# Optimization experiments

Measured on AMD Instinct MI355X. Metric: run time of the kernel, lower is better.

Reference implementation:

```python
import jax, jax.numpy as jnp
import numpy as np

KSIZE = 15
SIGMA = 3.0
PAD = KSIZE // 2


def _gauss_kernel2d():
    g = jnp.arange(KSIZE, dtype=jnp.float32) - KSIZE // 2
    g = jnp.exp(-(g ** 2) / (2.0 * SIGMA * SIGMA))
    g = g / g.sum()
    return g[:, None] * g[None, :]  # [15,15]


def _depthwise_blur(x, k2):
    # x: [B,C,H,W]; 15x15 Gaussian applied per channel (matches per-channel F.conv2d loop)
    C = x.shape[1]
    kernel = jnp.broadcast_to(k2[None, None], (C, 1, KSIZE, KSIZE))
    return jax.lax.conv_general_dilated(
        x, kernel, window_strides=(1, 1), padding=[(PAD, PAD), (PAD, PAD)],
        feature_group_count=C, dimension_numbers=("NCHW", "OIHW", "NCHW"))


def setup_inputs() -> dict:
    key = jax.random.key(0)
    B, C, H, W = 4, 3, 1024, 1024
    x = jax.random.uniform(key, (B, C, H, W), dtype=jnp.float32)
    f32 = lambda v: jnp.asarray(v, dtype=jnp.float32)
    return {
        "x": x,
        "gains": jnp.array([1.1, 1.0, 0.9], dtype=jnp.float32),
        "gamma": f32(0.9),
        "shadow_boost": f32(0.1),
        "highlight_reduce": f32(0.1),
        "brightness": f32(0.05),
        "contrast": f32(1.1),
        "enhance_amount": f32(0.8),
        "softness": f32(0.6),
        "intensity": f32(0.3),
        "rotation": f32(30.0),
        "hardness": f32(2.0),
    }


def reference(x, gains, gamma, shadow_boost, highlight_reduce, brightness,
              contrast, enhance_amount, softness, intensity, rotation, hardness):
    B, C, H, W = x.shape
    k2 = _gauss_kernel2d()

    # WhiteBalanceAdjustment
    x = x * gains.reshape(1, C, 1, 1)
    # ToneCurveAdjustment
    x = jnp.power(x, gamma)
    # ShadowHighlightEnhancement
    hi = jax.nn.sigmoid((x - 0.5) * 10.0)
    x = jnp.clip(x + shadow_boost * (1.0 - hi) - highlight_reduce * hi, 0.0, 1.0)
    # GlobalBrightnessContrastAdjustment
    x = jnp.clip(contrast * (x - 0.5) + 0.5 + brightness, 0.0, 1.0)
    # LocalContrastEnhancement
    local_mean = _depthwise_blur(x, k2)
    x = x + enhance_amount * (x - local_mean)
    # SoftnessFilter
    blurred = _depthwise_blur(x, k2)
    x = softness * blurred + (1.0 - softness) * x
    # GradientNDAdjustment
    ys = jnp.linspace(-1.0, 1.0, H, dtype=jnp.float32)
    xs = jnp.linspace(-1.0, 1.0, W, dtype=jnp.float32)
    grid_y, grid_x = jnp.meshgrid(ys, xs, indexing="ij")
    theta = rotation * (np.pi / 180.0)
    grid_rot = grid_x * jnp.cos(theta) + grid_y * jnp.sin(theta)
    mask = jax.nn.sigmoid(-hardness * grid_rot)[None, None]  # [1,1,H,W]
    x = jnp.clip(x * (1.0 - intensity * mask), 0.0, 1.0)

    return jnp.clip(x, 0.0, 1.0)
```

## Files before the change

### kernel.cpp

```cpp
#include <hip/hip_runtime.h>
#include <math.h>

#define HH 1024
#define WW 1024
#define NPLANES 12
#define PLANE (HH * WW)

#define TW 64
#define TH 64
#define RROWS 92
#define PA 96
#define PB 80
#define P1 80
#define PC 64

struct W15 { float w[15]; };

__device__ inline float chain1(float t, float gain, float gamma, float sb,
                               float hr, float br, float ct) {
    t = t * gain;
    t = __builtin_amdgcn_exp2f(gamma * __log2f(t));
    float hi = __fdividef(1.0f, 1.0f + __expf((0.5f - t) * 10.0f));
    t = t + sb * (1.0f - hi) - hr * hi;
    t = fminf(fmaxf(t, 0.0f), 1.0f);
    t = ct * (t - 0.5f) + 0.5f + br;
    return fminf(fmaxf(t, 0.0f), 1.0f);
}

__device__ inline float4 hdot4(const float* f, const W15& wk) {
    float4 o; float* po = (float*)&o;
#pragma unroll
    for (int j = 0; j < 4; ++j) {
        float a = 0.0f, b = 0.0f;
#pragma unroll
        for (int k = 0; k < 8; ++k)  a += wk.w[k] * f[j + 1 + k];
#pragma unroll
        for (int k = 8; k < 15; ++k) b += wk.w[k] * f[j + 1 + k];
        po[j] = a + b;
    }
    return o;
}

__device__ inline float dot15(const float* win, const W15& wk) {
    float a = 0.0f, b = 0.0f;
#pragma unroll
    for (int k = 0; k < 8; ++k)  a += wk.w[k] * win[k];
#pragma unroll
    for (int k = 8; k < 15; ++k) b += wk.w[k] * win[k];
    return a + b;
}

__device__ inline void tile_map(int& p, int& x0, int& y0, bool& edge) {
    int L = (blockIdx.z * gridDim.y + blockIdx.y) * gridDim.x + blockIdx.x;
    int xcd = L & 7;
    int t   = L >> 3;
    int g   = xcd * 384 + t;
    p = g >> 8;
    int w  = g & 255;
    int ty = w >> 4, tx = w & 15;
    x0 = tx * TW; y0 = ty * TH;
    edge = (tx == 0) || (tx == 15) || (ty == 0) || (ty == 15);
}

__global__ __launch_bounds__(256) void k_fused(
    const float* __restrict__ x, float* __restrict__ dst,
    const float* __restrict__ gains,
    const float* __restrict__ pg, const float* __restrict__ psb,
    const float* __restrict__ phr, const float* __restrict__ pbr,
    const float* __restrict__ pct, const float* __restrict__ penh,
    const float* __restrict__ psoft, const float* __restrict__ pint,
    const float* __restrict__ prot, const float* __restrict__ phard,
    W15 wk)
{
    __shared__ float A [RROWS * PA];
    __shared__ float Bb[RROWS * PB];

    int p, x0, y0; bool edge;
    tile_map(p, x0, y0, edge);
    const int tid = threadIdx.x;
    const int tx  = tid & 63;
    const int ty  = tid >> 6;

    const float* __restrict__ plane = x + (size_t)p * PLANE;
    const float gain  = gains[p % 3];
    const float gamma = *pg, sb = *psb, hr = *phr, br = *pbr, ct = *pct;

    if (!edge) {
        const float* base = plane + (size_t)(y0 - 14) * WW + (x0 - 16);
        auto do1 = [&](int c) {
            int r = c / 24, c4 = c % 24;
            float4 v = *(const float4*)(base + (size_t)r * WW + 4 * c4);
            float* pv = (float*)&v;
#pragma unroll
            for (int q = 0; q < 4; ++q)
                pv[q] = chain1(pv[q], gain, gamma, sb, hr, br, ct);
            *(float4*)&A[r * PA + ((c4 ^ (r & 7)) << 2)] = v;
        };
#pragma unroll
        for (int it = 0; it < 8; ++it) do1(tid + 256 * it);
        if (tid < 160) do1(tid + 2048);
    } else {
        auto do1e = [&](int c) {
            int r = c / 24, c4 = c % 24;
            int gy  = y0 - 14 + r;
            int gx0 = x0 - 16 + 4 * c4;
            float4 v = make_float4(0.f, 0.f, 0.f, 0.f);
            if ((unsigned)gy < HH) {
                const float* row = plane + (size_t)gy * WW;
                float* pv = (float*)&v;
                if (gx0 >= 0 && gx0 + 3 < WW) {
                    v = *(const float4*)(row + gx0);
#pragma unroll
                    for (int q = 0; q < 4; ++q)
                        pv[q] = chain1(pv[q], gain, gamma, sb, hr, br, ct);
                } else {
#pragma unroll
                    for (int q = 0; q < 4; ++q) {
                        int gx = gx0 + q;
                        if ((unsigned)gx < WW)
                            pv[q] = chain1(row[gx], gain, gamma, sb, hr, br, ct);
                    }
                }
            }
            *(float4*)&A[r * PA + ((c4 ^ (r & 7)) << 2)] = v;
        };
#pragma unroll
        for (int it = 0; it < 8; ++it) do1e(tid + 256 * it);
        if (tid < 160) do1e(tid + 2048);
    }
    __syncthreads();

    float cc[16];
#pragma unroll
    for (int j = 0; j < 16; ++j) {
        int rr = ty * 16 + j + 14;
        cc[j] = A[rr * PA + ((((tx >> 2) + 4) ^ (rr & 7)) << 2) + (tx & 3)];
    }
    {
        auto do2 = [&](int c) {
            int r = c / 20, j4 = c % 20;
            int rx = r & 7;
            float f[20];
#pragma unroll
            for (int i = 0; i < 5; ++i)
                *(float4*)&f[4 * i] =
                    *(const float4*)&A[r * PA + (((j4 + i) ^ rx) << 2)];
            *(float4*)&Bb[r * PB + 4 * j4] = hdot4(f, wk);
        };
#pragma unroll
        for (int it = 0; it < 7; ++it) do2(tid + 256 * it);
        if (tid < 48) do2(tid + 1792);
    }
    __syncthreads();

    float* B1 = A;
    if (tid < 240) {
        int j    = tid % 80;
        int band = tid / 80;
        int r1s  = band * 26;
        bool xin = (unsigned)(x0 - 8 + j) < WW;
        float win[15];
#pragma unroll
        for (int k = 0; k < 14; ++k) win[k] = Bb[(r1s + k) * PB + j];
#pragma unroll
        for (int jj = 0; jj < 26; ++jj) {
            win[14] = Bb[(r1s + jj + 14) * PB + j];
            float v = dot15(win, wk);
            if (edge) {
                int gy = y0 - 7 + r1s + jj;
                if (!((unsigned)gy < HH) || !xin) v = 0.0f;
            }
            B1[(r1s + jj) * P1 + j] = v;
#pragma unroll
            for (int k = 0; k < 14; ++k) win[k] = win[k + 1];
        }
    }
    __syncthreads();

    float bb[16];
#pragma unroll
    for (int j = 0; j < 16; ++j)
        bb[j] = B1[(ty * 16 + j + 7) * P1 + (tx + 8)];
    float* C = Bb;
    {
        auto do4 = [&](int c) {
            int r = c >> 4, j4 = c & 15;
            float f[20];
#pragma unroll
            for (int i = 0; i < 5; ++i)
                *(float4*)&f[4 * i] = *(const float4*)&B1[r * P1 + 4 * (j4 + i)];
            *(float4*)&C[r * PC + 4 * j4] = hdot4(f, wk);
        };
#pragma unroll
        for (int it = 0; it < 4; ++it) do4(tid + 256 * it);
        if (tid < 224) do4(tid + 1024);
    }
    __syncthreads();

    const float e     = *penh;
    const float s     = *psoft;
    const float inten = *pint;
    const float hard  = *phard;
    const float theta = (*prot) * 0.017453292519943295f;
    const float cth = __cosf(theta), sth = __sinf(theta);
    const int   gx    = x0 + tx;
    const float gbase = (-1.0f + 2.0f * (float)gx * (1.0f / (float)(WW - 1))) * cth;
    const float ce    = 1.0f + e;

    float win[15];
#pragma unroll
    for (int k = 0; k < 14; ++k) win[k] = C[(ty * 16 + k) * PC + tx];

    float* __restrict__ dstP = dst + (size_t)p * PLANE;
#pragma unroll
    for (int jj = 0; jj < 16; ++jj) {
        win[14] = C[(ty * 16 + jj + 14) * PC + tx];
        float B2  = dot15(win, wk);
        float x2c = ce * cc[jj] - e * bb[jj];
        float bx2 = ce * bb[jj] - e * B2;
        float v   = s * bx2 + (1.0f - s) * x2c;
        int   y   = y0 + ty * 16 + jj;
        float gyn = -1.0f + 2.0f * (float)y * (1.0f / (float)(HH - 1));
        float mask = __fdividef(1.0f, 1.0f + __expf(hard * (gbase + gyn * sth)));
        v = v * (1.0f - inten * mask);
        v = fminf(fmaxf(v, 0.0f), 1.0f);
        dstP[(size_t)y * WW + gx] = v;
#pragma unroll
        for (int k = 0; k < 14; ++k) win[k] = win[k + 1];
    }
}

extern "C" void kernel_launch(void* const* d_in, const int* in_sizes, int n_in,
                              void* d_out, int out_size, void* d_ws, size_t ws_size,
                              hipStream_t stream)
{
    const float* x       = (const float*)d_in[0];
    const float* gains   = (const float*)d_in[1];
    const float* p_gamma = (const float*)d_in[2];
    const float* p_sb    = (const float*)d_in[3];
    const float* p_hr    = (const float*)d_in[4];
    const float* p_br    = (const float*)d_in[5];
    const float* p_ct    = (const float*)d_in[6];
    const float* p_enh   = (const float*)d_in[7];
    const float* p_soft  = (const float*)d_in[8];
    const float* p_int   = (const float*)d_in[9];
    const float* p_rot   = (const float*)d_in[10];
    const float* p_hard  = (const float*)d_in[11];

    W15 wk;
    {
        double g[15], sum = 0.0;
        for (int i = 0; i < 15; ++i) { double d = (double)(i - 7); g[i] = exp(-d * d / 18.0); sum += g[i]; }
        for (int i = 0; i < 15; ++i) wk.w[i] = (float)(g[i] / sum);
    }

    dim3 grid(WW / TW, HH / TH, NPLANES);
    k_fused<<<grid, dim3(256), 0, stream>>>(
        x, (float*)d_out, gains, p_gamma, p_sb, p_hr, p_br, p_ct,
        p_enh, p_soft, p_int, p_rot, p_hard, wk);
}
```

Measured before the change: 202.6 us.

## Fuse input load with horizontal blur in registers and shrink LDS staging

Each thread now loads a 32-wide strip of a row straight from global memory, applies the tone chain and computes 16 horizontal blur outputs in registers. Only the horizontally blurred result goes to shared memory, so the full pre-blur tile is no longer staged there and one barrier disappears. The centre values are reloaded from global and the tone chain recomputed for them, and the second horizontal pass also processes 16 outputs per thread. Shared memory drops to one combined, swizzled buffer, which may raise occupancy. The cost is redundant global loads, repeated tone-chain evaluation on halo columns, and higher register pressure from the 32-float strips.

```diff
diff --git a/kernel.cpp b/kernel.cpp
--- a/kernel.cpp
+++ b/kernel.cpp
@@ -8,11 +8,9 @@
 
 #define TW 64
 #define TH 64
-#define RROWS 92
-#define PA 96
-#define PB 80
-#define P1 80
-#define PC 64
+#define RH 92
+#define RB 78
+#define PH 80
 
 struct W15 { float w[15]; };
 
@@ -27,18 +25,21 @@
     return fminf(fmaxf(t, 0.0f), 1.0f);
 }
 
-__device__ inline float4 hdot4(const float* f, const W15& wk) {
-    float4 o; float* po = (float*)&o;
-#pragma unroll
-    for (int j = 0; j < 4; ++j) {
+__device__ inline int hq(int r, int q) { return r * PH + ((q ^ (r & 3)) << 2); }
+__device__ inline int hs(int r, int j) {
+    return r * PH + ((((j >> 2) ^ (r & 3)) << 2) | (j & 3));
+}
+
+__device__ inline void dot16(const float* f, const W15& wk, float* o) {
+#pragma unroll
+    for (int j = 0; j < 16; ++j) {
         float a = 0.0f, b = 0.0f;
 #pragma unroll
         for (int k = 0; k < 8; ++k)  a += wk.w[k] * f[j + 1 + k];
 #pragma unroll
         for (int k = 8; k < 15; ++k) b += wk.w[k] * f[j + 1 + k];
-        po[j] = a + b;
-    }
-    return o;
+        o[j] = a + b;
+    }
 }
 
 __device__ inline float dot15(const float* win, const W15& wk) {
@@ -72,8 +73,9 @@
     const float* __restrict__ prot, const float* __restrict__ phard,
     W15 wk)
 {
-    __shared__ float A [RROWS * PA];
-    __shared__ float Bb[RROWS * PB];
+    __shared__ float lds[(RH + RB) * PH];
+    float* Hs  = lds;
+    float* B1s = lds + RH * PH;
 
     int p, x0, y0; bool edge;
     tile_map(p, x0, y0, edge);
@@ -85,120 +87,96 @@
     const float gain  = gains[p % 3];
     const float gamma = *pg, sb = *psb, hr = *phr, br = *pbr, ct = *pct;
 
-    if (!edge) {
-        const float* base = plane + (size_t)(y0 - 14) * WW + (x0 - 16);
-        auto do1 = [&](int c) {
-            int r = c / 24, c4 = c % 24;
-            float4 v = *(const float4*)(base + (size_t)r * WW + 4 * c4);
-            float* pv = (float*)&v;
-#pragma unroll
-            for (int q = 0; q < 4; ++q)
-                pv[q] = chain1(pv[q], gain, gamma, sb, hr, br, ct);
-            *(float4*)&A[r * PA + ((c4 ^ (r & 7)) << 2)] = v;
-        };
-#pragma unroll
-        for (int it = 0; it < 8; ++it) do1(tid + 256 * it);
-        if (tid < 160) do1(tid + 2048);
-    } else {
-        auto do1e = [&](int c) {
-            int r = c / 24, c4 = c % 24;
+#pragma unroll
+    for (int it = 0; it < 2; ++it) {
+        int u = tid + 256 * it;
+        if (u < RH * 5) {
+            int r = u / 5, s = u - 5 * r;
             int gy  = y0 - 14 + r;
-            int gx0 = x0 - 16 + 4 * c4;
-            float4 v = make_float4(0.f, 0.f, 0.f, 0.f);
-            if ((unsigned)gy < HH) {
-                const float* row = plane + (size_t)gy * WW;
-                float* pv = (float*)&v;
-                if (gx0 >= 0 && gx0 + 3 < WW) {
-                    v = *(const float4*)(row + gx0);
-#pragma unroll
-                    for (int q = 0; q < 4; ++q)
-                        pv[q] = chain1(pv[q], gain, gamma, sb, hr, br, ct);
-                } else {
-#pragma unroll
-                    for (int q = 0; q < 4; ++q) {
-                        int gx = gx0 + q;
-                        if ((unsigned)gx < WW)
-                            pv[q] = chain1(row[gx], gain, gamma, sb, hr, br, ct);
-                    }
+            int gxa = x0 + 16 * s - 16;
+            float f[32];
+            if (!edge) {
+                const float* rp = plane + (size_t)gy * WW + gxa;
+#pragma unroll
+                for (int i = 0; i < 8; ++i)
+                    *(float4*)&f[4 * i] = *(const float4*)(rp + 4 * i);
+#pragma unroll
+                for (int e2 = 1; e2 < 31; ++e2)
+                    f[e2] = chain1(f[e2], gain, gamma, sb, hr, br, ct);
+            } else {
+                bool rowin = (unsigned)gy < HH;
+                const float* rp = plane + (size_t)(rowin ? gy : 0) * WW;
+                f[0] = 0.0f; f[31] = 0.0f;
+#pragma unroll
+                for (int e2 = 1; e2 < 31; ++e2) {
+                    int gx2 = gxa + e2;
+                    float v = 0.0f;
+                    if (rowin && (unsigned)gx2 < WW)
+                        v = chain1(rp[gx2], gain, gamma, sb, hr, br, ct);
+                    f[e2] = v;
                 }
             }
-            *(float4*)&A[r * PA + ((c4 ^ (r & 7)) << 2)] = v;
-        };
-#pragma unroll
-        for (int it = 0; it < 8; ++it) do1e(tid + 256 * it);
-        if (tid < 160) do1e(tid + 2048);
+            float o[16];
+            dot16(f, wk, o);
+#pragma unroll
+            for (int qq = 0; qq < 4; ++qq)
+                *(float4*)&Hs[hq(r, 4 * s + qq)] = *(float4*)&o[4 * qq];
+        }
+    }
+
+    float cc[16];
+    {
+        const float* pc0 = plane + (size_t)(y0 + ty * 16) * WW + (x0 + tx);
+#pragma unroll
+        for (int jj = 0; jj < 16; ++jj) cc[jj] = pc0[(size_t)jj * WW];
+#pragma unroll
+        for (int jj = 0; jj < 16; ++jj)
+            cc[jj] = chain1(cc[jj], gain, gamma, sb, hr, br, ct);
     }
     __syncthreads();
 
-    float cc[16];
-#pragma unroll
-    for (int j = 0; j < 16; ++j) {
-        int rr = ty * 16 + j + 14;
-        cc[j] = A[rr * PA + ((((tx >> 2) + 4) ^ (rr & 7)) << 2) + (tx & 3)];
-    }
-    {
-        auto do2 = [&](int c) {
-            int r = c / 20, j4 = c % 20;
-            int rx = r & 7;
-            float f[20];
-#pragma unroll
-            for (int i = 0; i < 5; ++i)
-                *(float4*)&f[4 * i] =
-                    *(const float4*)&A[r * PA + (((j4 + i) ^ rx) << 2)];
-            *(float4*)&Bb[r * PB + 4 * j4] = hdot4(f, wk);
-        };
-#pragma unroll
-        for (int it = 0; it < 7; ++it) do2(tid + 256 * it);
-        if (tid < 48) do2(tid + 1792);
-    }
-    __syncthreads();
-
-    float* B1 = A;
     if (tid < 240) {
-        int j    = tid % 80;
-        int band = tid / 80;
-        int r1s  = band * 26;
+        int j = tid % 80, band = tid / 80;
+        int rb0 = 26 * band;
         bool xin = (unsigned)(x0 - 8 + j) < WW;
         float win[15];
 #pragma unroll
-        for (int k = 0; k < 14; ++k) win[k] = Bb[(r1s + k) * PB + j];
+        for (int k = 0; k < 14; ++k) win[k] = Hs[hs(rb0 + k, j)];
 #pragma unroll
         for (int jj = 0; jj < 26; ++jj) {
-            win[14] = Bb[(r1s + jj + 14) * PB + j];
+            win[14] = Hs[hs(rb0 + jj + 14, j)];
             float v = dot15(win, wk);
             if (edge) {
-                int gy = y0 - 7 + r1s + jj;
+                int gy = y0 - 7 + rb0 + jj;
                 if (!((unsigned)gy < HH) || !xin) v = 0.0f;
             }
-            B1[(r1s + jj) * P1 + j] = v;
+            B1s[hs(rb0 + jj, j)] = v;
 #pragma unroll
             for (int k = 0; k < 14; ++k) win[k] = win[k + 1];
         }
     }
     __syncthreads();
 
-    float bb[16];
-#pragma unroll
-    for (int j = 0; j < 16; ++j)
-        bb[j] = B1[(ty * 16 + j + 7) * P1 + (tx + 8)];
-    float* C = Bb;
-    {
-        auto do4 = [&](int c) {
-            int r = c >> 4, j4 = c & 15;
-            float f[20];
-#pragma unroll
-            for (int i = 0; i < 5; ++i)
-                *(float4*)&f[4 * i] = *(const float4*)&B1[r * P1 + 4 * (j4 + i)];
-            *(float4*)&C[r * PC + 4 * j4] = hdot4(f, wk);
-        };
-#pragma unroll
-        for (int it = 0; it < 4; ++it) do4(tid + 256 * it);
-        if (tid < 224) do4(tid + 1024);
+#pragma unroll
+    for (int it = 0; it < 2; ++it) {
+        int u = tid + 256 * it;
+        if (u < RB * 4) {
+            int rb = u >> 2, s = u & 3;
+            float f[32];
+#pragma unroll
+            for (int i = 0; i < 8; ++i)
+                *(float4*)&f[4 * i] = *(const float4*)&B1s[hq(rb, 4 * s + i)];
+            float o[16];
+            dot16(f, wk, o);
+#pragma unroll
+            for (int qq = 0; qq < 4; ++qq)
+                *(float4*)&Hs[hq(rb, 4 * s + qq)] = *(float4*)&o[4 * qq];
+        }
     }
     __syncthreads();
 
     const float e     = *penh;
-    const float s     = *psoft;
+    const float sf    = *psoft;
     const float inten = *pint;
     const float hard  = *phard;
     const float theta = (*prot) * 0.017453292519943295f;
@@ -207,18 +185,23 @@
     const float gbase = (-1.0f + 2.0f * (float)gx * (1.0f / (float)(WW - 1))) * cth;
     const float ce    = 1.0f + e;
 
+    float bb[16];
+#pragma unroll
+    for (int jj = 0; jj < 16; ++jj)
+        bb[jj] = B1s[hs(ty * 16 + jj + 7, tx + 8)];
+
     float win[15];
 #pragma unroll
-    for (int k = 0; k < 14; ++k) win[k] = C[(ty * 16 + k) * PC + tx];
+    for (int k = 0; k < 14; ++k) win[k] = Hs[hs(ty * 16 + k, tx)];
 
     float* __restrict__ dstP = dst + (size_t)p * PLANE;
 #pragma unroll
     for (int jj = 0; jj < 16; ++jj) {
-        win[14] = C[(ty * 16 + jj + 14) * PC + tx];
+        win[14] = Hs[hs(ty * 16 + jj + 14, tx)];
         float B2  = dot15(win, wk);
         float x2c = ce * cc[jj] - e * bb[jj];
         float bx2 = ce * bb[jj] - e * B2;
-        float v   = s * bx2 + (1.0f - s) * x2c;
+        float v   = sf * bx2 + (1.0f - sf) * x2c;
         int   y   = y0 + ty * 16 + jj;
         float gyn = -1.0f + 2.0f * (float)y * (1.0f / (float)(HH - 1));
         float mask = __fdividef(1.0f, 1.0f + __expf(hard * (gbase + gyn * sth)));
```

After: 220.6 us. 1.09x slower.
